# Optimization experiments

Measured on AMD Instinct MI355X. Metric: run time of the kernel, lower is better.

## Reference

```python
import jax, jax.numpy as jnp
import numpy as np

N_NODES = 100000
HIDDEN = 128
N_EDGES = 1000000


def setup_inputs() -> dict:
    key = jax.random.key(0)
    k1, k2, k3, k4 = jax.random.split(key, 4)
    z = jax.random.normal(k1, (N_NODES, HIDDEN), dtype=jnp.float32)
    edge_label_index = jax.random.randint(k2, (2, N_EDGES), 0, N_NODES, dtype=jnp.int64)
    # Kaiming-ish scaled init for the two Linear layers (lin1: 2H->H, lin2: H->1)
    W1 = jax.random.normal(k3, (2 * HIDDEN, HIDDEN), dtype=jnp.float32) / np.sqrt(2 * HIDDEN)
    b1 = jnp.zeros((HIDDEN,), dtype=jnp.float32)
    W2 = jax.random.normal(k4, (HIDDEN, 1), dtype=jnp.float32) / np.sqrt(HIDDEN)
    b2 = jnp.zeros((1,), dtype=jnp.float32)
    return {"z": z, "edge_label_index": edge_label_index, "W1": W1, "b1": b1, "W2": W2, "b2": b2}


def reference(z, edge_label_index, W1, b1, W2, b2):
    row, col = edge_label_index[0], edge_label_index[1]
    # gather endpoint embeddings and concat: [E, 2H]
    h = jnp.concatenate([z[row], z[col]], axis=-1)
    h = jax.nn.relu(h @ W1 + b1)          # [E, H]
    out = h @ W2 + b2                     # [E, 1]
    return out.reshape(-1)
```

## Files before the change

kernel.cpp:

```cpp
#include <hip/hip_runtime.h>
#include <hip/hip_bf16.h>
#include <stdint.h>

#define HIDDEN 128

typedef __attribute__((ext_vector_type(8))) short short8;
typedef __attribute__((ext_vector_type(4))) unsigned uint4v;
typedef __attribute__((ext_vector_type(4))) float float4v;
typedef __attribute__((ext_vector_type(2))) float float2v;
typedef __attribute__((ext_vector_type(2))) unsigned uint2v;

static __device__ __forceinline__ unsigned short f2bf(float f) {
    union { float f; unsigned u; } v; v.f = f;
    unsigned r = (v.u + 0x7FFFu + ((v.u >> 16) & 1u)) >> 16;
    return (unsigned short)r;
}

static __device__ __forceinline__ unsigned pack2bf(float f0, float f1) {
    unsigned u0 = __float_as_uint(f0) + 0x8000u;
    unsigned u1 = __float_as_uint(f1) + 0x8000u;
    return __builtin_amdgcn_perm(u1, u0, 0x07060302u);
}

static __device__ __forceinline__ short8 pack8(float4v lo, float4v hi) {
    uint4v u;
    u[0] = pack2bf(lo[0], lo[1]);
    u[1] = pack2bf(lo[2], lo[3]);
    u[2] = pack2bf(hi[0], hi[1]);
    u[3] = pack2bf(hi[2], hi[3]);
    return *(short8*)&u;
}

__global__ void prep_wt(const float* __restrict__ W1, const float* __restrict__ b1,
                        const float* __restrict__ W2,
                        unsigned short* __restrict__ Wt,
                        float* __restrict__ b1p, float* __restrict__ W2p) {
    int idx = blockIdx.x * blockDim.x + threadIdx.x;
    if (idx < 256 * 128) {
        int j = idx >> 7, k = idx & 127;
        float v = (j < 128) ? W1[k * 128 + j] : W1[(128 + k) * 128 + (j - 128)];
        Wt[idx] = f2bf(v);
    }
    if (idx < 128) {
        int m = idx >> 3, tt = idx & 7;
        int jj = tt * 16 + m;
        b1p[idx] = b1[jj];
        W2p[idx] = W2[jj];
    }
}

__global__ __launch_bounds__(512) void node_gemm(
        const float* __restrict__ z, const unsigned short* __restrict__ Wt,
        const float* __restrict__ b1p,
        unsigned char* __restrict__ Qi, float* __restrict__ sA, float* __restrict__ sB,
        int n_nodes) {
    __shared__ unsigned short Wl[2 * 128 * 128];

    int tid  = threadIdx.x;
    int lane = tid & 63;
    int wave = tid >> 6;
    int m    = lane & 15;
    int quad = lane >> 4;

    int nTiles   = (n_nodes + 15) >> 4;
    int tile     = blockIdx.x * 8 + wave;
    bool active  = tile < nTiles;
    int nodebase = tile * 16;
    int row      = nodebase + m;

    float4v zr[8];
    {
        bool ok = active && (row < n_nodes);
        const float* zp = z + (size_t)row * HIDDEN + quad * 8;
        #pragma unroll
        for (int s = 0; s < 4; ++s) {
            zr[2 * s]     = ok ? *(const float4v*)(zp + s * 32)     : (float4v)(0.0f);
            zr[2 * s + 1] = ok ? *(const float4v*)(zp + s * 32 + 4) : (float4v)(0.0f);
        }
    }

    #pragma unroll
    for (int i = 0; i < 8; ++i) {
        int chunk = tid + i * 512;
        int c  = chunk >> 4;
        int k0 = (chunk & 15) * 8;
        short8 v = *(const short8*)(Wt + chunk * 8);
        int off = c * 128 + k0;
        *(short8*)(Wl + (off ^ ((c & 7) << 3))) = v;
    }
    __syncthreads();
    if (!active) return;

    float4v b1a = *(const float4v*)(b1p + m * 8);
    float4v b1b = *(const float4v*)(b1p + m * 8 + 4);

    short8 a[4];
    #pragma unroll
    for (int s = 0; s < 4; ++s) a[s] = pack8(zr[2 * s], zr[2 * s + 1]);

    #pragma unroll
    for (int h = 0; h < 2; ++h) {
        float4v acc[8];
        #pragma unroll
        for (int t = 0; t < 8; ++t) acc[t] = (float4v)(0.0f);

        int swz = (m & 7) << 3;
        #pragma unroll
        for (int t = 0; t < 8; ++t) {
            int base = (h * 128 + t * 16 + m) * 128 + quad * 8;
            #pragma unroll
            for (int s = 0; s < 4; ++s) {
                short8 b = *(const short8*)(Wl + ((base + s * 32) ^ swz));
                acc[t] = __builtin_amdgcn_mfma_f32_16x16x32_bf16(a[s], b, acc[t], 0, 0, 0);
            }
        }

        float4v ba = (h == 0) ? b1a : (float4v)(0.0f);
        float4v bb = (h == 0) ? b1b : (float4v)(0.0f);
        float* sArr = (h == 0) ? sA : sB;

        #pragma unroll
        for (int r = 0; r < 4; ++r) {
            int node = nodebase + quad * 4 + r;
            float v[8];
            v[0] = acc[0][r] + ba[0]; v[1] = acc[1][r] + ba[1];
            v[2] = acc[2][r] + ba[2]; v[3] = acc[3][r] + ba[3];
            v[4] = acc[4][r] + bb[0]; v[5] = acc[5][r] + bb[1];
            v[6] = acc[6][r] + bb[2]; v[7] = acc[7][r] + bb[3];

            float amax = fabsf(v[0]);
            #pragma unroll
            for (int t = 1; t < 8; ++t) amax = fmaxf(amax, fabsf(v[t]));
            amax = fmaxf(amax, __shfl_xor(amax, 1));
            amax = fmaxf(amax, __shfl_xor(amax, 2));
            amax = fmaxf(amax, __shfl_xor(amax, 4));
            amax = fmaxf(amax, __shfl_xor(amax, 8));
            amax = fmaxf(amax, 1e-30f);

            float inv = 126.5f * __builtin_amdgcn_rcpf(amax);
            float s   = amax * (1.0f / 126.5f);

            unsigned d0 = 0, d1 = 0;
            #pragma unroll
            for (int t = 0; t < 4; ++t) {
                int q = (int)rintf(fmaf(v[t], inv, 128.0f));
                d0 |= ((unsigned)q & 255u) << (8 * t);
            }
            #pragma unroll
            for (int t = 0; t < 4; ++t) {
                int q = (int)rintf(fmaf(v[4 + t], inv, 128.0f));
                d1 |= ((unsigned)q & 255u) << (8 * t);
            }

            if (node < n_nodes) {
                uint2v pk; pk[0] = d0; pk[1] = d1;
                *(uint2v*)(Qi + (size_t)node * 256 + h * 128 + m * 8) = pk;
                if (m == 0) sArr[node] = s;
            }
        }
    }
}

static __device__ __forceinline__ float edge_dot8(uint2v u1, uint2v u2,
                                                  float a1, float a2,
                                                  const float2v* w2) {
    float offs = -128.0f * (a1 + a2);
    float2v off2; off2[0] = offs; off2[1] = offs;
    float2v a1v;  a1v[0] = a1;   a1v[1] = a1;
    float2v a2v;  a2v[0] = a2;   a2v[1] = a2;
    float2v acc2; acc2[0] = 0.0f; acc2[1] = 0.0f;
    #pragma unroll
    for (int d = 0; d < 2; ++d) {
        unsigned da = u1[d], db = u2[d];
        #pragma unroll
        for (int p = 0; p < 2; ++p) {
            float2v af, bf;
            af[0] = (float)((da >> (16 * p))     & 255u);
            af[1] = (float)((da >> (16 * p + 8)) & 255u);
            bf[0] = (float)((db >> (16 * p))     & 255u);
            bf[1] = (float)((db >> (16 * p + 8)) & 255u);
            float2v t = a2v * bf + off2;
            float2v s = a1v * af + t;
            s[0] = fmaxf(s[0], 0.0f);
            s[1] = fmaxf(s[1], 0.0f);
            acc2 = acc2 + s * w2[2 * d + p];
        }
    }
    return acc2[0] + acc2[1];
}

__global__ __launch_bounds__(256) void edge_kernel(
        const int* __restrict__ eli, const unsigned char* __restrict__ Qi,
        const float* __restrict__ sA, const float* __restrict__ sB,
        const float* __restrict__ W2p, const float* __restrict__ b2,
        float* __restrict__ out, int E) {
    int g      = threadIdx.x >> 4;
    int lane16 = threadIdx.x & 15;
    int j0     = lane16 * 8;

    float2v w2[4];
    #pragma unroll
    for (int k = 0; k < 4; ++k) w2[k] = ((const float2v*)(W2p + j0))[k];
    float bias2 = b2[0];

    int ebase = blockIdx.x * 128 + g * 8;

    int idx_r[8], idx_c[8];
    #pragma unroll
    for (int i = 0; i < 8; ++i) {
        int e = ebase + i;
        bool ok = e < E;
        idx_r[i] = ok ? eli[e]     : 0;
        idx_c[i] = ok ? eli[E + e] : 0;
    }

    uint2v u1[8], u2[8];
    #pragma unroll
    for (int i = 0; i < 8; ++i) {
        u1[i] = *(const uint2v*)(Qi + (size_t)idx_r[i] * 256 + j0);
        u2[i] = *(const uint2v*)(Qi + (size_t)idx_c[i] * 256 + 128 + j0);
    }
    float s1[8], s2[8];
    #pragma unroll
    for (int i = 0; i < 8; ++i) {
        s1[i] = sA[idx_r[i]];
        s2[i] = sB[idx_c[i]];
    }

    float res[8];
    #pragma unroll
    for (int i = 0; i < 8; ++i) {
        float acc = edge_dot8(u1[i], u2[i], s1[i], s2[i], w2);
        acc += __shfl_xor(acc, 1);
        acc += __shfl_xor(acc, 2);
        acc += __shfl_xor(acc, 4);
        acc += __shfl_xor(acc, 8);
        res[i] = acc + bias2;
    }

    if (lane16 == 0) {
        if (ebase + 8 <= E) {
            float4v r0, r1;
            r0[0] = res[0]; r0[1] = res[1]; r0[2] = res[2]; r0[3] = res[3];
            r1[0] = res[4]; r1[1] = res[5]; r1[2] = res[6]; r1[3] = res[7];
            *(float4v*)(out + ebase)     = r0;
            *(float4v*)(out + ebase + 4) = r1;
        } else {
            #pragma unroll
            for (int i = 0; i < 8; ++i)
                if (ebase + i < E) out[ebase + i] = res[i];
        }
    }
}

extern "C" void kernel_launch(void* const* d_in, const int* in_sizes, int n_in,
                              void* d_out, int out_size, void* d_ws, size_t ws_size,
                              hipStream_t stream) {
    const float* z   = (const float*)d_in[0];
    const int*   eli = (const int*)d_in[1];
    const float* W1  = (const float*)d_in[2];
    const float* b1  = (const float*)d_in[3];
    const float* W2  = (const float*)d_in[4];
    const float* b2  = (const float*)d_in[5];
    int n_nodes = in_sizes[0] / HIDDEN;
    int E       = in_sizes[1] / 2;
    float* out  = (float*)d_out;

    size_t off = 0;
    unsigned char* Qi  = (unsigned char*)d_ws;                 off += (size_t)n_nodes * 256;
    unsigned short* Wt = (unsigned short*)((char*)d_ws + off); off += 256 * 128 * 2;
    float* b1p = (float*)((char*)d_ws + off);                  off += 128 * 4;
    float* W2p = (float*)((char*)d_ws + off);                  off += 128 * 4;
    float* sA  = (float*)((char*)d_ws + off);                  off += (size_t)n_nodes * 4;
    float* sB  = (float*)((char*)d_ws + off);                  off += (size_t)n_nodes * 4;

    prep_wt<<<128, 256, 0, stream>>>(W1, b1, W2, Wt, b1p, W2p);

    int nTiles = (n_nodes + 15) / 16;
    node_gemm<<<(nTiles + 7) / 8, 512, 0, stream>>>(z, Wt, b1p, Qi, sA, sB, n_nodes);

    edge_kernel<<<(E + 127) / 128, 256, 0, stream>>>(eli, Qi, sA, sB, W2p, b2, out, E);
}
```

Before: 158.6 us.

## Bucket-sort edges by source node before gathering for locality

Adds a histogram and scatter pass that groups edges into 256 buckets by row index (512 nodes per bucket). The edge kernel then reads the reordered row/col pairs and writes each result back through the saved original edge id. The aim is to improve L2 locality of the row-side Qi/sA gathers. In exchange it adds two extra passes over the edge indices, atomics, and an extra 12 bytes per edge of workspace traffic, and the final output writes become scattered.

```diff
diff --git a/kernel.cpp b/kernel.cpp
--- a/kernel.cpp
+++ b/kernel.cpp
@@ -3,6 +3,7 @@
 #include <stdint.h>
 
 #define HIDDEN 128
+#define BSHIFT 9
 
 typedef __attribute__((ext_vector_type(8))) short short8;
 typedef __attribute__((ext_vector_type(4))) unsigned uint4v;
@@ -34,7 +35,8 @@
 __global__ void prep_wt(const float* __restrict__ W1, const float* __restrict__ b1,
                         const float* __restrict__ W2,
                         unsigned short* __restrict__ Wt,
-                        float* __restrict__ b1p, float* __restrict__ W2p) {
+                        float* __restrict__ b1p, float* __restrict__ W2p,
+                        unsigned* __restrict__ gHist) {
     int idx = blockIdx.x * blockDim.x + threadIdx.x;
     if (idx < 256 * 128) {
         int j = idx >> 7, k = idx & 127;
@@ -47,6 +49,7 @@
         b1p[idx] = b1[jj];
         W2p[idx] = W2[jj];
     }
+    if (gHist && idx < 512) gHist[idx] = 0;
 }
 
 __global__ __launch_bounds__(512) void node_gemm(
@@ -158,6 +161,63 @@
                 if (m == 0) sArr[node] = s;
             }
         }
+    }
+}
+
+__global__ __launch_bounds__(256) void edge_hist(
+        const int* __restrict__ eli, int E, unsigned* __restrict__ gHist) {
+    __shared__ unsigned lh[256];
+    lh[threadIdx.x] = 0;
+    __syncthreads();
+    for (int e = blockIdx.x * blockDim.x + threadIdx.x; e < E;
+         e += gridDim.x * blockDim.x)
+        atomicAdd(&lh[(unsigned)eli[e] >> BSHIFT], 1u);
+    __syncthreads();
+    unsigned v = lh[threadIdx.x];
+    if (v) atomicAdd(&gHist[threadIdx.x], v);
+}
+
+__global__ __launch_bounds__(256) void edge_scatter(
+        const int* __restrict__ eli, int E,
+        const unsigned* __restrict__ gHist, unsigned* __restrict__ gCur,
+        int2* __restrict__ rc, int* __restrict__ oid) {
+    __shared__ unsigned loff[256];
+    __shared__ unsigned lh[256];
+    __shared__ unsigned lbase[256];
+    int t = threadIdx.x;
+
+    unsigned h = gHist[t];
+    loff[t] = h;
+    __syncthreads();
+    #pragma unroll
+    for (int d = 1; d < 256; d <<= 1) {
+        unsigned x = (t >= d) ? loff[t - d] : 0u;
+        __syncthreads();
+        loff[t] += x;
+        __syncthreads();
+    }
+    unsigned excl = loff[t] - h;
+
+    lh[t] = 0;
+    __syncthreads();
+    int chunk = (E + gridDim.x - 1) / gridDim.x;
+    int e0 = blockIdx.x * chunk;
+    int e1 = min(e0 + chunk, E);
+    for (int e = e0 + t; e < e1; e += 256)
+        atomicAdd(&lh[(unsigned)eli[e] >> BSHIFT], 1u);
+    __syncthreads();
+    unsigned cnt = lh[t];
+    lbase[t] = excl + (cnt ? atomicAdd(&gCur[t], cnt) : 0u);
+    lh[t] = 0;
+    __syncthreads();
+    for (int e = e0 + t; e < e1; e += 256) {
+        int r = eli[e];
+        int b = (unsigned)r >> BSHIFT;
+        unsigned k = atomicAdd(&lh[b], 1u);
+        unsigned pos = lbase[b] + k;
+        int2 v; v.x = r; v.y = eli[E + e];
+        rc[pos] = v;
+        oid[pos] = e;
     }
 }
 
@@ -189,6 +249,59 @@
     return acc2[0] + acc2[1];
 }
 
+__global__ __launch_bounds__(256) void edge_kernel_sorted(
+        const int2* __restrict__ rc, const int* __restrict__ oid,
+        const unsigned char* __restrict__ Qi,
+        const float* __restrict__ sA, const float* __restrict__ sB,
+        const float* __restrict__ W2p, const float* __restrict__ b2,
+        float* __restrict__ out, int E) {
+    int g      = threadIdx.x >> 4;
+    int lane16 = threadIdx.x & 15;
+    int j0     = lane16 * 8;
+
+    float2v w2[4];
+    #pragma unroll
+    for (int k = 0; k < 4; ++k) w2[k] = ((const float2v*)(W2p + j0))[k];
+    float bias2 = b2[0];
+
+    int pbase = blockIdx.x * 128 + g * 8;
+
+    int idx_r[8], idx_c[8], id[8];
+    #pragma unroll
+    for (int i = 0; i < 8; ++i) {
+        int p = pbase + i;
+        bool ok = p < E;
+        int2 v = ok ? rc[p] : (int2){0, 0};
+        idx_r[i] = v.x;
+        idx_c[i] = v.y;
+        id[i]    = ok ? oid[p] : 0;
+    }
+
+    uint2v u1[8], u2[8];
+    #pragma unroll
+    for (int i = 0; i < 8; ++i) {
+        u1[i] = *(const uint2v*)(Qi + (size_t)idx_r[i] * 256 + j0);
+        u2[i] = *(const uint2v*)(Qi + (size_t)idx_c[i] * 256 + 128 + j0);
+    }
+    float s1[8], s2[8];
+    #pragma unroll
+    for (int i = 0; i < 8; ++i) {
+        s1[i] = sA[idx_r[i]];
+        s2[i] = sB[idx_c[i]];
+    }
+
+    #pragma unroll
+    for (int i = 0; i < 8; ++i) {
+        float acc = edge_dot8(u1[i], u2[i], s1[i], s2[i], w2);
+        acc += __shfl_xor(acc, 1);
+        acc += __shfl_xor(acc, 2);
+        acc += __shfl_xor(acc, 4);
+        acc += __shfl_xor(acc, 8);
+        if (lane16 == 0 && pbase + i < E)
+            out[id[i]] = acc + bias2;
+    }
+}
+
 __global__ __launch_bounds__(256) void edge_kernel(
         const int* __restrict__ eli, const unsigned char* __restrict__ Qi,
         const float* __restrict__ sA, const float* __restrict__ sB,
@@ -274,10 +387,25 @@
     float* sA  = (float*)((char*)d_ws + off);                  off += (size_t)n_nodes * 4;
     float* sB  = (float*)((char*)d_ws + off);                  off += (size_t)n_nodes * 4;
 
-    prep_wt<<<128, 256, 0, stream>>>(W1, b1, W2, Wt, b1p, W2p);
+    int2* rcBuf = (int2*)((char*)d_ws + off);                  size_t off2 = off + (size_t)E * 8;
+    int*  oidBuf = (int*)((char*)d_ws + off2);                 off2 += (size_t)E * 4;
+    unsigned* gHist = (unsigned*)((char*)d_ws + off2);         off2 += 512 * 4;
+    unsigned* gCur  = gHist + 256;
+
+    bool useSort = (ws_size >= off2) && (n_nodes <= (256 << BSHIFT));
+
+    prep_wt<<<128, 256, 0, stream>>>(W1, b1, W2, Wt, b1p, W2p,
+                                     useSort ? gHist : (unsigned*)nullptr);
 
     int nTiles = (n_nodes + 15) / 16;
     node_gemm<<<(nTiles + 7) / 8, 512, 0, stream>>>(z, Wt, b1p, Qi, sA, sB, n_nodes);
 
-    edge_kernel<<<(E + 127) / 128, 256, 0, stream>>>(eli, Qi, sA, sB, W2p, b2, out, E);
-}
+    if (useSort) {
+        edge_hist<<<256, 256, 0, stream>>>(eli, E, gHist);
+        edge_scatter<<<256, 256, 0, stream>>>(eli, E, gHist, gCur, rcBuf, oidBuf);
+        edge_kernel_sorted<<<(E + 127) / 128, 256, 0, stream>>>(
+            rcBuf, oidBuf, Qi, sA, sB, W2p, b2, out, E);
+    } else {
+        edge_kernel<<<(E + 127) / 128, 256, 0, stream>>>(eli, Qi, sA, sB, W2p, b2, out, E);
+    }
+}
```

Result: slower. 205.0 us (+29.2%).
